# Optimization experiments

Hardware: AMD Instinct MI355X
Metric: run time of the kernel (lower is better)

Reference implementation:

```python
import jax, jax.numpy as jnp
import numpy as np

N_GRAPHS = 2048
NODES_PER_GRAPH = 64
N = N_GRAPHS * NODES_PER_GRAPH  # 131072 total nodes
D = 256
A = 32
HEADS = 2
NEG = -1e9
EPS = 1e-20


def setup_inputs() -> dict:
    key = jax.random.key(0)
    ks = jax.random.split(key, 9)
    values = jax.random.normal(ks[0], (N, D), dtype=jnp.float32)
    # balanced ragged layout: sorted segment ids, NODES_PER_GRAPH nodes per graph
    indices = (jnp.arange(N, dtype=jnp.int32) // NODES_PER_GRAPH).astype(jnp.int32)
    n_nodes = jnp.full((N_GRAPHS,), NODES_PER_GRAPH, dtype=jnp.int32)
    action_type_mask = jax.random.uniform(ks[1], (N, A)) > 0.2
    action_arity_mask = jax.random.uniform(ks[2], (N, A)) > 0.2
    a_act = jax.random.randint(ks[3], (N_GRAPHS,), 0, A)
    a_node = jnp.arange(N_GRAPHS) * NODES_PER_GRAPH + jax.random.randint(ks[4], (N_GRAPHS,), 0, NODES_PER_GRAPH)
    a = jnp.stack([a_act, a_node], axis=1).astype(jnp.int32)
    W_node = jax.random.normal(ks[5], (1, D), dtype=jnp.float32) * 0.05
    W_agn = jax.random.normal(ks[6], (A, D), dtype=jnp.float32) * 0.05
    W_nga = jax.random.normal(ks[7], (A, D), dtype=jnp.float32) * 0.05
    W_q = jax.random.normal(ks[8], (A * HEADS, D), dtype=jnp.float32) * 0.05
    return {"a": a, "values": values, "indices": indices,
            "action_type_mask": action_type_mask, "action_arity_mask": action_arity_mask,
            "n_nodes": n_nodes, "W_node": W_node, "W_agn": W_agn, "W_nga": W_nga, "W_q": W_q}


def mask_logits(logits, mask):
    return jnp.where(mask, logits, NEG)


def segment_softmax(logits, seg, n_seg):
    # softmax over nodes within each segment, independently per trailing dim
    m = jax.ops.segment_max(logits, seg, num_segments=n_seg)
    z = jnp.exp(logits - m[seg])
    s = jax.ops.segment_sum(z, seg, num_segments=n_seg)
    return z / s[seg]


def reference(a, values, indices, action_type_mask, action_arity_mask, n_nodes,
              W_node, W_agn, W_nga, W_q):
    n_g = n_nodes.shape[0]
    segsum = lambda x: jax.ops.segment_sum(x, indices, num_segments=n_g)

    node_logits = (values @ W_node.T).squeeze(-1)          # [N]
    agn_logits = values @ W_agn.T                           # [N, A]
    nga_logits = values @ W_nga.T                           # [N, A]

    agn_mask = action_type_mask
    nga_mask = jnp.logical_and(action_arity_mask, action_type_mask)

    # marginalize: p(a) = sum_n p(n) * p(a|n)
    p_n = segment_softmax(node_logits, indices, n_g)        # [N]
    p_a_given_n = jax.nn.softmax(mask_logits(agn_logits, agn_mask), axis=-1)  # [N, A]
    p_a = segsum(p_n[:, None] * p_a_given_n)                # [G, A]

    # p(n|a): segment softmax over nodes per action
    p_n__a = segment_softmax(mask_logits(nga_logits, nga_mask), indices, n_g)  # [N, A]

    # critic: mean over heads of per-(node, action) Q
    q = (values @ W_q.T).reshape(-1, HEADS, A).mean(axis=1)  # [N, A]
    value = jnp.sum(p_a * segsum(p_n__a * q), axis=-1)       # [G]

    # eval_action_then_node: logprob / entropy of the joint (action, node)
    a_act, a_node = a[:, 0], a[:, 1]
    g = jnp.arange(n_g)
    logprob = jnp.log(p_a[g, a_act] + EPS) + jnp.log(p_n__a[a_node, a_act] + EPS)  # [G]

    ent_a = -jnp.sum(p_a * jnp.log(p_a + EPS), axis=-1)      # [G]
    h_n = -segsum(p_n__a * jnp.log(p_n__a + EPS))            # [G, A]
    entropy = ent_a + jnp.sum(p_a * h_n, axis=-1)            # [G]

    return (logprob, entropy, value, p_a, p_n__a)
```

## Files before the change

kernel.cpp:

```cpp
#include <hip/hip_runtime.h>


#define NG   2048
#define NEGV -1000000000.0f
#define EPSV 1e-20f

struct WS {
  int flag;
  int pad[63];
  float Wall[8 * 112 * 32];
};

__global__ void prep_kernel(const unsigned char* __restrict__ atm,
                            const float* __restrict__ Wn,
                            const float* __restrict__ Wagn,
                            const float* __restrict__ Wnga,
                            const float* __restrict__ Wq,
                            WS* __restrict__ ws)
{
  const int t = threadIdx.x;
  const int b = blockIdx.x;
  if (b == 0) {
    __shared__ int s_off, s_max;
    if (t == 0) { s_off = 0; s_max = 0; }
    __syncthreads();
    int loc_off = 0, loc_max = 0;
    for (int i = t; i < 4096; i += 256) {
      int v = atm[i];
      loc_max = max(loc_max, v);
      if ((i & 3) != 0 && v != 0) loc_off = 1;
    }
    if (loc_off) atomicOr(&s_off, 1);
    atomicMax(&s_max, loc_max);
    __syncthreads();
    if (t == 0) ws->flag = (s_max > 1) ? 1 : (s_off ? 0 : 1);
  }
  for (int e = b * 256 + t; e < 112 * 256; e += 64 * 256) {
    int ro = e >> 8, k = e & 255;
    float w = 0.f;
    if (ro == 0)       w = Wn[k];
    else if (ro < 33)  w = Wagn[(ro - 1) * 256 + k];
    else if (ro < 65)  w = Wnga[(ro - 33) * 256 + k];
    else if (ro < 97)  w = 0.5f * (Wq[(ro - 65) * 256 + k] + Wq[(ro - 33) * 256 + k]);
    ws->Wall[(k >> 5) * 3584 + ro * 32 + (k & 31)] = w;
  }
}

__device__ __forceinline__ void load_chunk(float4 (&vX)[8], const float4* __restrict__ vrow) {
  #pragma unroll
  for (int k4 = 0; k4 < 8; ++k4) vX[k4] = vrow[k4];
}

__device__ __forceinline__ void compute_chunk(const float4 (&vX)[8],
                                              const float* __restrict__ wt,
                                              float (&acc)[25], int rcnt) {
  #pragma unroll
  for (int r = 0; r < 25; ++r) {
    if (r < rcnt) {
      const float* wr = wt + r * 32;
      float s = acc[r];
      #pragma unroll
      for (int k4 = 0; k4 < 8; ++k4) {
        s = fmaf(vX[k4].x, wr[(k4 << 2) + 0], s);
        s = fmaf(vX[k4].y, wr[(k4 << 2) + 1], s);
        s = fmaf(vX[k4].z, wr[(k4 << 2) + 2], s);
        s = fmaf(vX[k4].w, wr[(k4 << 2) + 3], s);
      }
      acc[r] = s;
    }
  }
}

__global__ __launch_bounds__(256, 4) void policy_kernel(
    const int* __restrict__ a_in,
    const float* __restrict__ values,
    const void* __restrict__ atm,
    const void* __restrict__ aam,
    const WS* __restrict__ ws,
    float* __restrict__ out)
{
  __shared__ float sm[6724];

  const int t  = threadIdx.x;
  const int g  = blockIdx.x;
  const int n  = t & 63;
  const int wvu = __builtin_amdgcn_readfirstlane(t >> 6);
  const int rbase = wvu ? wvu * 24 + 1 : 0;
  const int rcnt  = wvu ? 24 : 25;

  float acc[25];
  #pragma unroll
  for (int r = 0; r < 25; ++r) acc[r] = 0.f;

  const float4* vrow = (const float4*)(values + (size_t)g * 16384 + (size_t)n * 256);
  const float*  wbase = ws->Wall + rbase * 32;

  float4 vA[8], vB[8];
  load_chunk(vA, vrow);

  #pragma unroll 1
  for (int kt = 0; kt < 8; kt += 2) {
    load_chunk(vB, vrow + (kt + 1) * 8);
    compute_chunk(vA, wbase + kt * 3584, acc, rcnt);
    if (kt < 6) load_chunk(vA, vrow + (kt + 2) * 8);
    compute_chunk(vB, wbase + (kt + 1) * 3584, acc, rcnt);
  }

  float* Out = sm;
  #pragma unroll
  for (int r = 0; r < 25; ++r)
    if (r < rcnt) Out[(rbase + r) * 65 + n] = acc[r];
  __syncthreads();

  float* pn   = sm + 6308;
  float* papt = sm + 6372;
  float* pa   = sm + 6628;
  float* segq = sm + 6660;
  float* hn   = sm + 6692;

  const int f4 = ws->flag;
  const size_t mb = (size_t)g * 2048;
  auto mget = [&](const void* p, size_t idx) -> bool {
    return f4 ? (((const int*)p)[idx] != 0)
              : (((const unsigned char*)p)[idx] != 0);
  };

  if (t < 64) {
    float x = Out[t];
    float m = x;
    #pragma unroll
    for (int s = 32; s > 0; s >>= 1) m = fmaxf(m, __shfl_xor(m, s));
    float z = __expf(x - m);
    float su = z;
    #pragma unroll
    for (int s = 32; s > 0; s >>= 1) su += __shfl_xor(su, s);
    pn[t] = z / su;
  }
  __syncthreads();

  {
    const int aA = t & 31, grp = t >> 5;
    float part = 0.f;
    for (int j = 0; j < 8; ++j) {
      int nn = grp * 8 + j;
      bool mk = mget(atm, mb + (size_t)nn * 32 + aA);
      float l = mk ? Out[(1 + aA) * 65 + nn] : NEGV;
      float m = l;
      #pragma unroll
      for (int s = 16; s > 0; s >>= 1) m = fmaxf(m, __shfl_xor(m, s));
      float z = __expf(l - m);
      float su = z;
      #pragma unroll
      for (int s = 16; s > 0; s >>= 1) su += __shfl_xor(su, s);
      part += pn[nn] * (z / su);
    }
    papt[grp * 32 + aA] = part;
  }

  {
    const int a2 = t >> 3, r = t & 7;
    float lj[8];
    float m = -3.4e38f;
    #pragma unroll
    for (int j = 0; j < 8; ++j) {
      int nn = r * 8 + j;
      size_t mi = mb + (size_t)nn * 32 + a2;
      bool mk = mget(atm, mi) && mget(aam, mi);
      float l = mk ? Out[(33 + a2) * 65 + nn] : NEGV;
      lj[j] = l;
      m = fmaxf(m, l);
    }
    #pragma unroll
    for (int s = 4; s > 0; s >>= 1) m = fmaxf(m, __shfl_xor(m, s));
    float su = 0.f;
    #pragma unroll
    for (int j = 0; j < 8; ++j) { lj[j] = __expf(lj[j] - m); su += lj[j]; }
    #pragma unroll
    for (int s = 4; s > 0; s >>= 1) su += __shfl_xor(su, s);
    float inv = 1.f / su;
    float hq = 0.f, pq = 0.f;
    #pragma unroll
    for (int j = 0; j < 8; ++j) {
      int nn = r * 8 + j;
      float p = lj[j] * inv;
      Out[(33 + a2) * 65 + nn] = p;
      hq -= p * __logf(p + EPSV);
      pq = fmaf(p, Out[(65 + a2) * 65 + nn], pq);
    }
    #pragma unroll
    for (int s = 4; s > 0; s >>= 1) { hq += __shfl_xor(hq, s); pq += __shfl_xor(pq, s); }
    if (r == 0) { segq[a2] = pq; hn[a2] = hq; }
  }
  __syncthreads();

  if (t < 32) {
    float s0 = 0.f;
    #pragma unroll
    for (int gq = 0; gq < 8; ++gq) s0 += papt[gq * 32 + t];
    pa[t] = s0;
    out[6144 + g * 32 + t] = s0;
    float v1 = s0 * segq[t];
    float e1 = -s0 * __logf(s0 + EPSV);
    float e2 = s0 * hn[t];
    #pragma unroll
    for (int s = 16; s > 0; s >>= 1) {
      v1 += __shfl_xor(v1, s);
      e1 += __shfl_xor(e1, s);
      e2 += __shfl_xor(e2, s);
    }
    if (t == 0) {
      out[4096 + g] = v1;
      out[2048 + g] = e1 + e2;
      int act = a_in[g * 2 + 0];
      int anl = a_in[g * 2 + 1] - g * 64;
      out[g] = __logf(pa[act] + EPSV) + __logf(Out[(33 + act) * 65 + anl] + EPSV);
    }
  }
  const size_t ob = 71680 + (size_t)g * 2048;
  #pragma unroll
  for (int i = 0; i < 8; ++i) {
    int e = t + (i << 8);
    out[ob + e] = Out[(33 + (e & 31)) * 65 + (e >> 5)];
  }
}

extern "C" void kernel_launch(void* const* d_in, const int* in_sizes, int n_in,
                              void* d_out, int out_size, void* d_ws, size_t ws_size,
                              hipStream_t stream)
{
  const int*   a_in   = (const int*)d_in[0];
  const float* values = (const float*)d_in[1];
  const void*  atm    = d_in[3];
  const void*  aam    = d_in[4];
  const float* Wn     = (const float*)d_in[6];
  const float* Wagn   = (const float*)d_in[7];
  const float* Wnga   = (const float*)d_in[8];
  const float* Wq     = (const float*)d_in[9];
  WS*    ws  = (WS*)d_ws;
  float* out = (float*)d_out;

  hipLaunchKernelGGL(prep_kernel, dim3(64), dim3(256), 0, stream,
                     (const unsigned char*)atm, Wn, Wagn, Wnga, Wq, ws);
  hipLaunchKernelGGL(policy_kernel, dim3(NG), dim3(256), 0, stream,
                     a_in, values, atm, aam, ws, out);
}
```

Measured before the change: 346.2 us.

## Replace FP32 FMA projection with split-bf16 MFMA (3-term hi/lo) matmul

```diff
diff --git a/kernel.cpp b/kernel.cpp
--- a/kernel.cpp
+++ b/kernel.cpp
@@ -5,10 +5,15 @@
 #define NEGV -1000000000.0f
 #define EPSV 1e-20f
 
+typedef __attribute__((ext_vector_type(8))) short bf16x8;
+typedef __attribute__((ext_vector_type(4))) float f32x4;
+typedef __attribute__((ext_vector_type(4))) unsigned int u32x4;
+
 struct WS {
   int flag;
   int pad[63];
-  float Wall[8 * 112 * 32];
+  unsigned short Ahi[8 * 7 * 64 * 8];
+  unsigned short Alo[8 * 7 * 64 * 8];
 };
 
 __global__ void prep_kernel(const unsigned char* __restrict__ atm,
@@ -35,40 +40,55 @@
     __syncthreads();
     if (t == 0) ws->flag = (s_max > 1) ? 1 : (s_off ? 0 : 1);
   }
-  for (int e = b * 256 + t; e < 112 * 256; e += 64 * 256) {
-    int ro = e >> 8, k = e & 255;
+  for (int e = b * 256 + t; e < 28672; e += 64 * 256) {
+    int kb  = e / 3584;
+    int rem = e - kb * 3584;
+    int mt  = rem >> 9;
+    int le  = rem & 511;
+    int lane = le >> 3, j = le & 7;
+    int row = mt * 16 + (lane & 15);
+    int k   = kb * 32 + ((lane >> 4) << 2) + (j & 3) + ((j >> 2) << 4);
     float w = 0.f;
-    if (ro == 0)       w = Wn[k];
-    else if (ro < 33)  w = Wagn[(ro - 1) * 256 + k];
-    else if (ro < 65)  w = Wnga[(ro - 33) * 256 + k];
-    else if (ro < 97)  w = 0.5f * (Wq[(ro - 65) * 256 + k] + Wq[(ro - 33) * 256 + k]);
-    ws->Wall[(k >> 5) * 3584 + ro * 32 + (k & 31)] = w;
-  }
-}
-
-__device__ __forceinline__ void load_chunk(float4 (&vX)[8], const float4* __restrict__ vrow) {
-  #pragma unroll
-  for (int k4 = 0; k4 < 8; ++k4) vX[k4] = vrow[k4];
-}
-
-__device__ __forceinline__ void compute_chunk(const float4 (&vX)[8],
-                                              const float* __restrict__ wt,
-                                              float (&acc)[25], int rcnt) {
-  #pragma unroll
-  for (int r = 0; r < 25; ++r) {
-    if (r < rcnt) {
-      const float* wr = wt + r * 32;
-      float s = acc[r];
-      #pragma unroll
-      for (int k4 = 0; k4 < 8; ++k4) {
-        s = fmaf(vX[k4].x, wr[(k4 << 2) + 0], s);
-        s = fmaf(vX[k4].y, wr[(k4 << 2) + 1], s);
-        s = fmaf(vX[k4].z, wr[(k4 << 2) + 2], s);
-        s = fmaf(vX[k4].w, wr[(k4 << 2) + 3], s);
-      }
-      acc[r] = s;
-    }
-  }
+    if (row == 0)       w = Wn[k];
+    else if (row < 33)  w = Wagn[(row - 1) * 256 + k];
+    else if (row < 65)  w = Wnga[(row - 33) * 256 + k];
+    else if (row < 97)  w = 0.5f * (Wq[(row - 65) * 256 + k] + Wq[(row - 33) * 256 + k]);
+    unsigned int ub = __float_as_uint(w);
+    unsigned short hi = (unsigned short)(ub >> 16);
+    float lof = w - __uint_as_float(ub & 0xFFFF0000u);
+    unsigned short lo = (unsigned short)(__float_as_uint(lof) >> 16);
+    ws->Ahi[e] = hi;
+    ws->Alo[e] = lo;
+  }
+}
+
+__device__ __forceinline__ void split_bf16(const float4& fa, const float4& fb,
+                                           bf16x8& bh, bf16x8& bl)
+{
+  unsigned int ax = __float_as_uint(fa.x), ay = __float_as_uint(fa.y);
+  unsigned int az = __float_as_uint(fa.z), aw = __float_as_uint(fa.w);
+  unsigned int bx = __float_as_uint(fb.x), by = __float_as_uint(fb.y);
+  unsigned int bz = __float_as_uint(fb.z), bw = __float_as_uint(fb.w);
+  u32x4 H;
+  H.x = (ax >> 16) | (ay & 0xFFFF0000u);
+  H.y = (az >> 16) | (aw & 0xFFFF0000u);
+  H.z = (bx >> 16) | (by & 0xFFFF0000u);
+  H.w = (bz >> 16) | (bw & 0xFFFF0000u);
+  float lax = fa.x - __uint_as_float(ax & 0xFFFF0000u);
+  float lay = fa.y - __uint_as_float(ay & 0xFFFF0000u);
+  float laz = fa.z - __uint_as_float(az & 0xFFFF0000u);
+  float law = fa.w - __uint_as_float(aw & 0xFFFF0000u);
+  float lbx = fb.x - __uint_as_float(bx & 0xFFFF0000u);
+  float lby = fb.y - __uint_as_float(by & 0xFFFF0000u);
+  float lbz = fb.z - __uint_as_float(bz & 0xFFFF0000u);
+  float lbw = fb.w - __uint_as_float(bw & 0xFFFF0000u);
+  u32x4 L;
+  L.x = (__float_as_uint(lax) >> 16) | (__float_as_uint(lay) & 0xFFFF0000u);
+  L.y = (__float_as_uint(laz) >> 16) | (__float_as_uint(law) & 0xFFFF0000u);
+  L.z = (__float_as_uint(lbx) >> 16) | (__float_as_uint(lby) & 0xFFFF0000u);
+  L.w = (__float_as_uint(lbz) >> 16) | (__float_as_uint(lbw) & 0xFFFF0000u);
+  bh = __builtin_bit_cast(bf16x8, H);
+  bl = __builtin_bit_cast(bf16x8, L);
 }
 
 __global__ __launch_bounds__(256, 4) void policy_kernel(
@@ -83,33 +103,56 @@
 
   const int t  = threadIdx.x;
   const int g  = blockIdx.x;
-  const int n  = t & 63;
-  const int wvu = __builtin_amdgcn_readfirstlane(t >> 6);
-  const int rbase = wvu ? wvu * 24 + 1 : 0;
-  const int rcnt  = wvu ? 24 : 25;
-
-  float acc[25];
+  const int l  = t & 63;
+  const int nt = __builtin_amdgcn_readfirstlane(t >> 6);
+  const int col = l & 15;
+  const int h   = l >> 4;
+
+  f32x4 acc[7];
   #pragma unroll
-  for (int r = 0; r < 25; ++r) acc[r] = 0.f;
-
-  const float4* vrow = (const float4*)(values + (size_t)g * 16384 + (size_t)n * 256);
-  const float*  wbase = ws->Wall + rbase * 32;
-
-  float4 vA[8], vB[8];
-  load_chunk(vA, vrow);
-
+  for (int mt = 0; mt < 7; ++mt) acc[mt] = f32x4{0.f, 0.f, 0.f, 0.f};
+
+  const float4* vbase = (const float4*)(values + (size_t)g * 16384 +
+                                        (size_t)(nt * 16 + col) * 256);
+  const u32x4* Ah = (const u32x4*)ws->Ahi;
+  const u32x4* Al = (const u32x4*)ws->Alo;
+
+  auto compute = [&](int kb, const float4& fa, const float4& fb) {
+    bf16x8 bh, bl;
+    split_bf16(fa, fb, bh, bl);
+    #pragma unroll
+    for (int mt = 0; mt < 7; ++mt) {
+      int idx = (kb * 7 + mt) * 64 + l;
+      bf16x8 ah = __builtin_bit_cast(bf16x8, Ah[idx]);
+      bf16x8 al = __builtin_bit_cast(bf16x8, Al[idx]);
+      acc[mt] = __builtin_amdgcn_mfma_f32_16x16x32_bf16(ah, bh, acc[mt], 0, 0, 0);
+      acc[mt] = __builtin_amdgcn_mfma_f32_16x16x32_bf16(ah, bl, acc[mt], 0, 0, 0);
+      acc[mt] = __builtin_amdgcn_mfma_f32_16x16x32_bf16(al, bh, acc[mt], 0, 0, 0);
+    }
+  };
+
+  float4 fa0 = vbase[h], fb0 = vbase[4 + h];
   #pragma unroll 1
-  for (int kt = 0; kt < 8; kt += 2) {
-    load_chunk(vB, vrow + (kt + 1) * 8);
-    compute_chunk(vA, wbase + kt * 3584, acc, rcnt);
-    if (kt < 6) load_chunk(vA, vrow + (kt + 2) * 8);
-    compute_chunk(vB, wbase + (kt + 1) * 3584, acc, rcnt);
+  for (int kb = 0; kb < 8; kb += 2) {
+    float4 fa1 = vbase[(kb + 1) * 8 + h];
+    float4 fb1 = vbase[(kb + 1) * 8 + 4 + h];
+    compute(kb, fa0, fb0);
+    if (kb < 6) {
+      fa0 = vbase[(kb + 2) * 8 + h];
+      fb0 = vbase[(kb + 2) * 8 + 4 + h];
+    }
+    compute(kb + 1, fa1, fb1);
   }
 
   float* Out = sm;
   #pragma unroll
-  for (int r = 0; r < 25; ++r)
-    if (r < rcnt) Out[(rbase + r) * 65 + n] = acc[r];
+  for (int mt = 0; mt < 7; ++mt) {
+    #pragma unroll
+    for (int r = 0; r < 4; ++r) {
+      int row = mt * 16 + h * 4 + r;
+      if (row < 97) Out[row * 65 + nt * 16 + col] = acc[mt][r];
+    }
+  }
   __syncthreads();
 
   float* pn   = sm + 6308;
@@ -144,11 +187,11 @@
     for (int j = 0; j < 8; ++j) {
       int nn = grp * 8 + j;
       bool mk = mget(atm, mb + (size_t)nn * 32 + aA);
-      float l = mk ? Out[(1 + aA) * 65 + nn] : NEGV;
-      float m = l;
+      float l2 = mk ? Out[(1 + aA) * 65 + nn] : NEGV;
+      float m = l2;
       #pragma unroll
       for (int s = 16; s > 0; s >>= 1) m = fmaxf(m, __shfl_xor(m, s));
-      float z = __expf(l - m);
+      float z = __expf(l2 - m);
       float su = z;
       #pragma unroll
       for (int s = 16; s > 0; s >>= 1) su += __shfl_xor(su, s);
@@ -166,9 +209,9 @@
       int nn = r * 8 + j;
       size_t mi = mb + (size_t)nn * 32 + a2;
       bool mk = mget(atm, mi) && mget(aam, mi);
-      float l = mk ? Out[(33 + a2) * 65 + nn] : NEGV;
-      lj[j] = l;
-      m = fmaxf(m, l);
+      float l2 = mk ? Out[(33 + a2) * 65 + nn] : NEGV;
+      lj[j] = l2;
+      m = fmaxf(m, l2);
     }
     #pragma unroll
     for (int s = 4; s > 0; s >>= 1) m = fmaxf(m, __shfl_xor(m, s));
```

After: 289.7 us. -16.3%, faster.
